# Optimization experiments

Hardware: AMD Instinct MI355X
Metric: run time of the kernel (lower is better)

Reference implementation:

```python
import jax, jax.numpy as jnp
import numpy as np

N = 50000
E = 800000
EP = 200000
IN_C = 128
HID = 128


def setup_inputs() -> dict:
    key = jax.random.key(0)
    ks = jax.random.split(key, 10)
    x = jax.random.normal(ks[0], (N, IN_C), dtype=jnp.float32)
    edge_index = jax.random.randint(ks[1], (2, E), 0, N, dtype=jnp.int64)
    pred_edges = jax.random.randint(ks[2], (2, EP), 0, N, dtype=jnp.int64)
    s_in = 1.0 / np.sqrt(IN_C)
    s_h = 1.0 / np.sqrt(HID)
    W1l = jax.random.normal(ks[3], (IN_C, HID), dtype=jnp.float32) * s_in
    W1r = jax.random.normal(ks[4], (IN_C, HID), dtype=jnp.float32) * s_in
    b1 = jnp.zeros((HID,), dtype=jnp.float32)
    W2l = jax.random.normal(ks[5], (HID, HID), dtype=jnp.float32) * s_h
    W2r = jax.random.normal(ks[6], (HID, HID), dtype=jnp.float32) * s_h
    b2 = jnp.zeros((HID,), dtype=jnp.float32)
    return {"x": x, "W1l": W1l, "b1": b1, "W1r": W1r,
            "W2l": W2l, "b2": b2, "W2r": W2r,
            "edge_index": edge_index, "pred_edges": pred_edges}


def _sage_conv(h, Wl, b, Wr, src, dst, n_nodes):
    # PyG SAGEConv (aggr='mean'): out = lin_l(mean_j x_j) + lin_r(x_i)
    msg = h[src]                                              # (E, D) gather
    agg = jax.ops.segment_sum(msg, dst, num_segments=n_nodes)  # (N, D) scatter-add
    deg = jax.ops.segment_sum(jnp.ones((src.shape[0],), h.dtype), dst,
                              num_segments=n_nodes)
    agg = agg / jnp.maximum(deg, 1.0)[:, None]                # mean (0 for isolated)
    return agg @ Wl + b + h @ Wr


def reference(x, W1l, b1, W1r, W2l, b2, W2r, edge_index, pred_edges):
    n_nodes = x.shape[0]
    src, dst = edge_index[0], edge_index[1]
    h = jax.nn.relu(_sage_conv(x, W1l, b1, W1r, src, dst, n_nodes))
    z = _sage_conv(h, W2l, b2, W2r, src, dst, n_nodes)
    ps, pd = pred_edges[0], pred_edges[1]
    return jnp.sum(z[ps] * z[pd], axis=-1)  # (E_pred,) logits
```

## Files before the change

kernel.cpp:

```cpp
#include <hip/hip_runtime.h>

#define D 128

typedef __attribute__((ext_vector_type(8))) short short8;
typedef __attribute__((ext_vector_type(4))) float f32x4;

__device__ inline unsigned int f2bf_bits(float f) {
    unsigned int u = __float_as_uint(f);
    return (u + 0x7FFFu + ((u >> 16) & 1u)) >> 16;
}

__device__ inline float bfhi(unsigned int u) { return __uint_as_float(u << 16); }
__device__ inline float bflo(unsigned int u) { return __uint_as_float(u & 0xffff0000u); }

__global__ __launch_bounds__(256) void prep_kernel(
    const float* __restrict__ x,
    const float* __restrict__ W1l, const float* __restrict__ W1r,
    const float* __restrict__ W2l, const float* __restrict__ W2r,
    const int* __restrict__ dst, int E,
    unsigned short* __restrict__ xbf, unsigned short* __restrict__ xlo,
    unsigned short* __restrict__ h1, unsigned short* __restrict__ l1,
    unsigned short* __restrict__ h2, unsigned short* __restrict__ l2,
    int n4, int ncast, int* __restrict__ chist2, int* __restrict__ csrpad)
{
    __shared__ int h[256];
    const int b = blockIdx.x;
    const int t = threadIdx.x;
    if (b < ncast) {
        int i = b * 256 + t;
        if (i >= n4) return;
        f32x4 v = *(const f32x4*)(x + (size_t)i * 4);
        ushort4 oh, ol;
        {
            unsigned int hb; float hf;
            hb = f2bf_bits(v.x); hf = __uint_as_float(hb << 16);
            oh.x = (unsigned short)hb; ol.x = (unsigned short)f2bf_bits(v.x - hf);
            hb = f2bf_bits(v.y); hf = __uint_as_float(hb << 16);
            oh.y = (unsigned short)hb; ol.y = (unsigned short)f2bf_bits(v.y - hf);
            hb = f2bf_bits(v.z); hf = __uint_as_float(hb << 16);
            oh.z = (unsigned short)hb; ol.z = (unsigned short)f2bf_bits(v.z - hf);
            hb = f2bf_bits(v.w); hf = __uint_as_float(hb << 16);
            oh.w = (unsigned short)hb; ol.w = (unsigned short)f2bf_bits(v.w - hf);
        }
        *(ushort4*)(xbf + (size_t)i * 4) = oh;
        *(ushort4*)(xlo + (size_t)i * 4) = ol;
    } else if (b < ncast + 256) {
        int gidx = (b - ncast) * 256 + t;
        int sel = gidx >> 15;
        int idx = gidx & 32767;
        int tt = idx >> 12;
        int ks = (idx >> 9) & 7;
        int lane = (idx >> 3) & 63;
        int j = idx & 7;
        int qq = lane >> 4, r16 = lane & 15;
        int k = ks * 32 + qq * 8 + j;
        int c = tt * 16 + r16;
        const float* Wl = sel ? W2l : W1l;
        const float* Wr = sel ? W2r : W1r;
        float v = (k < 128) ? Wl[k * 128 + c] : Wr[(k - 128) * 128 + c];
        unsigned int hb = f2bf_bits(v);
        float hf = __uint_as_float(hb << 16);
        unsigned int l = f2bf_bits(v - hf);
        (sel ? h2 : h1)[idx] = (unsigned short)hb;
        (sel ? l2 : l1)[idx] = (unsigned short)l;
    } else if (b < ncast + 512) {
        const int cb = b - ncast - 256;
        h[t] = 0;
        __syncthreads();
        for (int e = cb * 256 + t; e < E; e += 65536)
            atomicAdd(&h[dst[e] >> 8], 1);
        __syncthreads();
        chist2[cb * 256 + t] = h[t];
    } else {
        if (t < 32) csrpad[t] = 0;
    }
}

__global__ __launch_bounds__(256) void scan256_kernel(const int* __restrict__ chist2,
                                                      int* __restrict__ cbase,
                                                      int* __restrict__ gcur) {
    __shared__ int wsum[4];
    const int t = threadIdx.x, lane = t & 63, wv = t >> 6;
    int v = 0;
#pragma unroll 8
    for (int b = 0; b < 256; ++b) v += chist2[b * 256 + t];
    int s = v;
#pragma unroll
    for (int o = 1; o < 64; o <<= 1) {
        int u = __shfl_up(s, o, 64);
        if (lane >= o) s += u;
    }
    if (lane == 63) wsum[wv] = s;
    __syncthreads();
    int add = 0;
    for (int w = 0; w < wv; ++w) add += wsum[w];
    cbase[t + 1] = s + add;
    if (t == 0) cbase[0] = 0;
    gcur[t] = s + add - v;
}

#define CCHUNK 4096
__global__ __launch_bounds__(256) void coarse_scatter_kernel(
    const int* __restrict__ src, const int* __restrict__ dst,
    int* __restrict__ gcur, unsigned int* __restrict__ centries, int E)
{
    __shared__ int h[256];
    __shared__ int base[256];
    __shared__ unsigned int stage[CCHUNK];
    const int t = threadIdx.x;
    const int e0 = blockIdx.x * CCHUNK;
    h[t] = 0;
    __syncthreads();
#pragma unroll
    for (int i = 0; i < 16; ++i) {
        int e = e0 + i * 256 + t;
        unsigned int u = 0xFFFFFFFFu;
        if (e < E) {
            int d = dst[e];
            int s = src[e];
            int b = d >> 8;
            u = ((unsigned)b << 24) | ((unsigned)s << 8) | (unsigned)(d & 255);
            atomicAdd(&h[b], 1);
        }
        stage[i * 256 + t] = u;
    }
    __syncthreads();
    base[t] = atomicAdd(&gcur[t], h[t]);
    __syncthreads();
    h[t] = 0;
    __syncthreads();
#pragma unroll
    for (int i = 0; i < 16; ++i) {
        unsigned int u = stage[i * 256 + t];
        if (u != 0xFFFFFFFFu) {
            int b = u >> 24;
            int r = atomicAdd(&h[b], 1);
            centries[base[b] + r] = u & 0x00FFFFFFu;
        }
    }
}

#define DCAP 8192
__global__ __launch_bounds__(256) void fine_bucket_kernel(
    const unsigned int* __restrict__ centries,
    const int* __restrict__ cbase,
    int* __restrict__ offo, int* __restrict__ csr, int N, int E)
{
    __shared__ int h[256], ex[256], wsum[4];
    __shared__ int stg[DCAP];
    const int t = threadIdx.x, lane = t & 63, wv = t >> 6;
    const int b = blockIdx.x;
    const int s0 = cbase[b];
    const int cnt = cbase[b + 1] - s0;
    h[t] = 0;
    __syncthreads();
    for (int i = t; i < cnt; i += 256)
        atomicAdd(&h[centries[s0 + i] & 255], 1);
    __syncthreads();
    int v = h[t], s = v;
#pragma unroll
    for (int o = 1; o < 64; o <<= 1) {
        int u = __shfl_up(s, o, 64);
        if (lane >= o) s += u;
    }
    if (lane == 63) wsum[wv] = s;
    __syncthreads();
    int add = 0;
    for (int w = 0; w < wv; ++w) add += wsum[w];
    const int exc = s + add - v;
    ex[t] = exc;
    const int dg = b * 256 + t;
    if (dg < N) offo[dg] = s0 + exc;
    if (b == 0 && t == 0) offo[N] = E;
    h[t] = 0;
    __syncthreads();
    if (cnt <= DCAP) {
        for (int i = t; i < cnt; i += 256) {
            unsigned int u = centries[s0 + i];
            int dl = u & 255;
            int r = atomicAdd(&h[dl], 1);
            stg[ex[dl] + r] = (int)(u >> 8);
        }
        __syncthreads();
        for (int i = t; i < cnt; i += 256)
            csr[s0 + i] = stg[i];
    } else {
        for (int i = t; i < cnt; i += 256) {
            unsigned int u = centries[s0 + i];
            int dl = u & 255;
            int r = atomicAdd(&h[dl], 1);
            csr[s0 + ex[dl] + r] = (int)(u >> 8);
        }
    }
}

__global__ __launch_bounds__(256, 4) void fused_sage_kernel(
    const unsigned short* __restrict__ featbf,
    const int* __restrict__ off,
    const int* __restrict__ csr,
    const unsigned short* __restrict__ self_hi,
    const unsigned short* __restrict__ self_lo,
    const unsigned short* __restrict__ wpk_hi,
    const unsigned short* __restrict__ wpk_lo,
    const float* __restrict__ bias,
    unsigned short* __restrict__ out_hi,
    unsigned short* __restrict__ out_lo,
    int do_relu)
{
    __shared__ unsigned short AHs[4][64][8];
    __shared__ unsigned short ALs[4][64][8];
    __shared__ unsigned short outs_hi[16][128];
    __shared__ unsigned short outs_lo[16][128];

    const int w = threadIdx.x >> 6;
    const int l = threadIdx.x & 63;
    const int tile = blockIdx.x;
    const int n0w = tile * 16;

    const int gn = l >> 2;
    const int q2 = l & 3;
    const int gnode = n0w + gn;
    const int start = off[gnode];
    const int end   = off[gnode + 1];
    const unsigned short* fb = featbf + w * 32 + q2 * 8;

    float ga[8] = {0.f, 0.f, 0.f, 0.f, 0.f, 0.f, 0.f, 0.f};

#define ACC(rv)                                                         \
    { ga[0] += bfhi(rv.x); ga[1] += bflo(rv.x);                         \
      ga[2] += bfhi(rv.y); ga[3] += bflo(rv.y);                         \
      ga[4] += bfhi(rv.z); ga[5] += bflo(rv.z);                         \
      ga[6] += bfhi(rv.w); ga[7] += bflo(rv.w); }

    const uint4 zero4 = {0u, 0u, 0u, 0u};
    if (start < end) {
        int4 ix = *(const int4*)(csr + start);
        uint4 c0 = *(const uint4*)(fb + (size_t)ix.x * D);
        uint4 c1 = *(const uint4*)(fb + (size_t)ix.y * D);
        uint4 c2 = *(const uint4*)(fb + (size_t)ix.z * D);
        uint4 c3 = *(const uint4*)(fb + (size_t)ix.w * D);
        for (int e = start; e < end; e += 4) {
            int4 ixn = *(const int4*)(csr + e + 4);
            uint4 n0 = *(const uint4*)(fb + (size_t)ixn.x * D);
            uint4 n1 = *(const uint4*)(fb + (size_t)ixn.y * D);
            uint4 n2 = *(const uint4*)(fb + (size_t)ixn.z * D);
            uint4 n3 = *(const uint4*)(fb + (size_t)ixn.w * D);
            if (e + 1 >= end) c1 = zero4;
            if (e + 2 >= end) c2 = zero4;
            if (e + 3 >= end) c3 = zero4;
            ACC(c0) ACC(c1) ACC(c2) ACC(c3)
            c0 = n0; c1 = n1; c2 = n2; c3 = n3;
        }
    }
#undef ACC

    {
        const float dinv = 1.0f / (float)max(end - start, 1);
        short8 hi8, lo8;
#pragma unroll
        for (int c = 0; c < 8; ++c) {
            float v = ga[c] * dinv;
            unsigned int hb = f2bf_bits(v);
            hi8[c] = (short)hb;
            lo8[c] = (short)f2bf_bits(v - __uint_as_float(hb << 16));
        }
        *(short8*)&AHs[w][q2 * 16 + gn][0] = hi8;
        *(short8*)&ALs[w][q2 * 16 + gn][0] = lo8;
    }
    __syncthreads();

    const int q = l >> 4, r16 = l & 15;
    const int mnode = n0w + r16;
    f32x4 acc0 = {0.f, 0.f, 0.f, 0.f};
    f32x4 acc1 = {0.f, 0.f, 0.f, 0.f};
    const unsigned short* sph = self_hi + (size_t)mnode * D + q * 8;
    const unsigned short* spl = self_lo + (size_t)mnode * D + q * 8;
    const unsigned short* bh0 = wpk_hi + (size_t)(2 * w) * 4096 + l * 8;
    const unsigned short* bl0 = wpk_lo + (size_t)(2 * w) * 4096 + l * 8;

#pragma unroll
    for (int ks = 0; ks < 8; ++ks) {
        short8 AH, AL;
        if (ks < 4) {
            AH = *(const short8*)&AHs[ks][l][0];
            AL = *(const short8*)&ALs[ks][l][0];
        } else {
            AH = *(const short8*)(sph + (ks - 4) * 32);
            AL = *(const short8*)(spl + (ks - 4) * 32);
        }
        short8 BH0 = *(const short8*)(bh0 + ks * 512);
        short8 BL0 = *(const short8*)(bl0 + ks * 512);
        short8 BH1 = *(const short8*)(bh0 + 4096 + ks * 512);
        short8 BL1 = *(const short8*)(bl0 + 4096 + ks * 512);
        acc0 = __builtin_amdgcn_mfma_f32_16x16x32_bf16(AH, BH0, acc0, 0, 0, 0);
        acc0 = __builtin_amdgcn_mfma_f32_16x16x32_bf16(AL, BH0, acc0, 0, 0, 0);
        acc0 = __builtin_amdgcn_mfma_f32_16x16x32_bf16(AH, BL0, acc0, 0, 0, 0);
        acc1 = __builtin_amdgcn_mfma_f32_16x16x32_bf16(AH, BH1, acc1, 0, 0, 0);
        acc1 = __builtin_amdgcn_mfma_f32_16x16x32_bf16(AL, BH1, acc1, 0, 0, 0);
        acc1 = __builtin_amdgcn_mfma_f32_16x16x32_bf16(AH, BL1, acc1, 0, 0, 0);
    }

    {
        const float bv0 = bias[32 * w + r16];
        const float bv1 = bias[32 * w + 16 + r16];
#pragma unroll
        for (int r = 0; r < 4; ++r) {
            float v0 = acc0[r] + bv0;
            float v1 = acc1[r] + bv1;
            if (do_relu) { v0 = fmaxf(v0, 0.f); v1 = fmaxf(v1, 0.f); }
            const int row = q * 4 + r;
            unsigned int h0 = f2bf_bits(v0);
            unsigned int h1 = f2bf_bits(v1);
            outs_hi[row][32 * w + r16] = (unsigned short)h0;
            outs_hi[row][32 * w + 16 + r16] = (unsigned short)h1;
            outs_lo[row][32 * w + r16] =
                (unsigned short)f2bf_bits(v0 - __uint_as_float(h0 << 16));
            outs_lo[row][32 * w + 16 + r16] =
                (unsigned short)f2bf_bits(v1 - __uint_as_float(h1 << 16));
        }
    }
    __syncthreads();
    {
        const int tid = threadIdx.x;
        short8 vh = *(short8*)(&outs_hi[0][0] + tid * 8);
        *(short8*)(out_hi + (size_t)n0w * D + tid * 8) = vh;
        if (out_lo) {
            short8 vl = *(short8*)(&outs_lo[0][0] + tid * 8);
            *(short8*)(out_lo + (size_t)n0w * D + tid * 8) = vl;
        }
    }
}

__global__ __launch_bounds__(256) void pred_kernel(const unsigned short* __restrict__ zbf,
                                                   const int* __restrict__ ps,
                                                   const int* __restrict__ pd,
                                                   float* __restrict__ out, int EP) {
    int idx = blockIdx.x * 256 + threadIdx.x;
    int e = idx >> 4;
    if (e >= EP) return;
    int L = idx & 15;
    const unsigned short* fb = zbf + (size_t)L * 8;
    uint4 ra = *(const uint4*)(fb + (size_t)ps[e] * D);
    uint4 rb = *(const uint4*)(fb + (size_t)pd[e] * D);
    float p = bfhi(ra.x) * bfhi(rb.x) + bflo(ra.x) * bflo(rb.x)
            + bfhi(ra.y) * bfhi(rb.y) + bflo(ra.y) * bflo(rb.y)
            + bfhi(ra.z) * bfhi(rb.z) + bflo(ra.z) * bflo(rb.z)
            + bfhi(ra.w) * bfhi(rb.w) + bflo(ra.w) * bflo(rb.w);
#pragma unroll
    for (int off = 8; off > 0; off >>= 1) p += __shfl_xor(p, off, 16);
    if (L == 0) out[e] = p;
}

extern "C" void kernel_launch(void* const* d_in, const int* in_sizes, int n_in,
                              void* d_out, int out_size, void* d_ws, size_t ws_size,
                              hipStream_t stream) {
    const float* x   = (const float*)d_in[0];
    const float* W1l = (const float*)d_in[1];
    const float* b1  = (const float*)d_in[2];
    const float* W1r = (const float*)d_in[3];
    const float* W2l = (const float*)d_in[4];
    const float* b2  = (const float*)d_in[5];
    const float* W2r = (const float*)d_in[6];
    const int* edge_index = (const int*)d_in[7];
    const int* pred_edges = (const int*)d_in[8];
    float* out = (float*)d_out;

    const int N  = in_sizes[0] / D;
    const int E  = in_sizes[7] / 2;
    const int EP = in_sizes[8] / 2;

    const int* src = edge_index;
    const int* dst = edge_index + E;
    const int* ps  = pred_edges;
    const int* pd  = pred_edges + EP;

    int* chist2  = (int*)d_ws;
    int* cbase   = chist2 + 65536;
    int* gcur    = cbase + 272;
    int* off     = gcur + 256;
    unsigned int* centries = (unsigned int*)(off + 50016);
    int* csr     = (int*)(centries + E);
    unsigned short* w1_hi = (unsigned short*)(csr + E + 32 + 48);
    unsigned short* w1_lo = w1_hi + 32768;
    unsigned short* w2_hi = w1_lo + 32768;
    unsigned short* w2_lo = w2_hi + 32768;
    unsigned short* xbf   = w2_lo + 32768;
    unsigned short* xlo   = xbf + (size_t)N * D;
    unsigned short* hbf   = xlo + (size_t)N * D;
    unsigned short* hlo   = hbf + (size_t)N * D;
    unsigned short* zbf   = hlo + (size_t)N * D;

    const int n4 = N * D / 4;
    const int ncast = (n4 + 255) / 256;
    const int ntiles = N / 16;
    const int nbC = (E + CCHUNK - 1) / CCHUNK;
    const int nbD = (N + 255) / 256;
    const int nblk_pred = (EP * 16 + 255) / 256;

    prep_kernel<<<ncast + 513, 256, 0, stream>>>(x, W1l, W1r, W2l, W2r, dst, E,
                                                 xbf, xlo, w1_hi, w1_lo, w2_hi, w2_lo,
                                                 n4, ncast, chist2, csr + E);

    scan256_kernel<<<1, 256, 0, stream>>>(chist2, cbase, gcur);
    coarse_scatter_kernel<<<nbC, 256, 0, stream>>>(src, dst, gcur, centries, E);
    fine_bucket_kernel<<<nbD, 256, 0, stream>>>(centries, cbase, off, csr, N, E);

    fused_sage_kernel<<<ntiles, 256, 0, stream>>>(xbf, off, csr, xbf, xlo,
                                                  w1_hi, w1_lo, b1, hbf, hlo, 1);
    fused_sage_kernel<<<ntiles, 256, 0, stream>>>(hbf, off, csr, hbf, hlo,
                                                  w2_hi, w2_lo, b2, zbf,
                                                  (unsigned short*)nullptr, 0);
    pred_kernel<<<nblk_pred, 256, 0, stream>>>(zbf, ps, pd, out, EP);
}
```

Measured before the change: 241.3 us.

## Sort nodes by degree to balance neighbor-aggregation work within tiles

```diff
diff --git a/kernel.cpp b/kernel.cpp
--- a/kernel.cpp
+++ b/kernel.cpp
@@ -21,7 +21,8 @@
     unsigned short* __restrict__ xbf, unsigned short* __restrict__ xlo,
     unsigned short* __restrict__ h1, unsigned short* __restrict__ l1,
     unsigned short* __restrict__ h2, unsigned short* __restrict__ l2,
-    int n4, int ncast, int* __restrict__ chist2, int* __restrict__ csrpad)
+    int n4, int ncast, int* __restrict__ chist2, int* __restrict__ csrpad,
+    int* __restrict__ dhist)
 {
     __shared__ int h[256];
     const int b = blockIdx.x;
@@ -72,6 +73,7 @@
         __syncthreads();
         chist2[cb * 256 + t] = h[t];
     } else {
+        dhist[t] = 0;
         if (t < 32) csrpad[t] = 0;
     }
 }
@@ -144,7 +146,8 @@
 __global__ __launch_bounds__(256) void fine_bucket_kernel(
     const unsigned int* __restrict__ centries,
     const int* __restrict__ cbase,
-    int* __restrict__ offo, int* __restrict__ csr, int N, int E)
+    int* __restrict__ offo, int* __restrict__ csr,
+    int* __restrict__ deg, int* __restrict__ dhist, int N, int E)
 {
     __shared__ int h[256], ex[256], wsum[4];
     __shared__ int stg[DCAP];
@@ -158,6 +161,11 @@
         atomicAdd(&h[centries[s0 + i] & 255], 1);
     __syncthreads();
     int v = h[t], s = v;
+    const int dg = b * 256 + t;
+    if (dg < N) {
+        deg[dg] = v;
+        atomicAdd(&dhist[min(v, 255)], 1);
+    }
 #pragma unroll
     for (int o = 1; o < 64; o <<= 1) {
         int u = __shfl_up(s, o, 64);
@@ -169,7 +177,6 @@
     for (int w = 0; w < wv; ++w) add += wsum[w];
     const int exc = s + add - v;
     ex[t] = exc;
-    const int dg = b * 256 + t;
     if (dg < N) offo[dg] = s0 + exc;
     if (b == 0 && t == 0) offo[N] = E;
     h[t] = 0;
@@ -194,10 +201,39 @@
     }
 }
 
+__global__ __launch_bounds__(256) void dscan_kernel(const int* __restrict__ dhist,
+                                                    int* __restrict__ dcur) {
+    __shared__ int wsum[4];
+    const int t = threadIdx.x, lane = t & 63, wv = t >> 6;
+    int v = dhist[t];
+    int s = v;
+#pragma unroll
+    for (int o = 1; o < 64; o <<= 1) {
+        int u = __shfl_up(s, o, 64);
+        if (lane >= o) s += u;
+    }
+    if (lane == 63) wsum[wv] = s;
+    __syncthreads();
+    int add = 0;
+    for (int w = 0; w < wv; ++w) add += wsum[w];
+    dcur[t] = s + add - v;
+}
+
+__global__ __launch_bounds__(256) void dperm_kernel(const int* __restrict__ deg,
+                                                    int* __restrict__ dcur,
+                                                    int* __restrict__ perm, int N) {
+    int n = blockIdx.x * 256 + threadIdx.x;
+    if (n >= N) return;
+    int d = min(deg[n], 255);
+    int pos = atomicAdd(&dcur[d], 1);
+    perm[pos] = n;
+}
+
 __global__ __launch_bounds__(256, 4) void fused_sage_kernel(
     const unsigned short* __restrict__ featbf,
     const int* __restrict__ off,
     const int* __restrict__ csr,
+    const int* __restrict__ perm,
     const unsigned short* __restrict__ self_hi,
     const unsigned short* __restrict__ self_lo,
     const unsigned short* __restrict__ wpk_hi,
@@ -219,7 +255,7 @@
 
     const int gn = l >> 2;
     const int q2 = l & 3;
-    const int gnode = n0w + gn;
+    const int gnode = perm[n0w + gn];
     const int start = off[gnode];
     const int end   = off[gnode + 1];
     const unsigned short* fb = featbf + w * 32 + q2 * 8;
@@ -270,7 +306,7 @@
     __syncthreads();
 
     const int q = l >> 4, r16 = l & 15;
-    const int mnode = n0w + r16;
+    const int mnode = perm[n0w + r16];
     f32x4 acc0 = {0.f, 0.f, 0.f, 0.f};
     f32x4 acc1 = {0.f, 0.f, 0.f, 0.f};
     const unsigned short* sph = self_hi + (size_t)mnode * D + q * 8;
@@ -322,11 +358,13 @@
     __syncthreads();
     {
         const int tid = threadIdx.x;
-        short8 vh = *(short8*)(&outs_hi[0][0] + tid * 8);
-        *(short8*)(out_hi + (size_t)n0w * D + tid * 8) = vh;
+        const int row = tid >> 4, ch = tid & 15;
+        const int dn = perm[n0w + row];
+        short8 vh = *(short8*)(&outs_hi[row][ch * 8]);
+        *(short8*)(out_hi + (size_t)dn * D + ch * 8) = vh;
         if (out_lo) {
-            short8 vl = *(short8*)(&outs_lo[0][0] + tid * 8);
-            *(short8*)(out_lo + (size_t)n0w * D + tid * 8) = vl;
+            short8 vl = *(short8*)(&outs_lo[row][ch * 8]);
+            *(short8*)(out_lo + (size_t)dn * D + ch * 8) = vl;
         }
     }
 }
@@ -378,7 +416,11 @@
     int* cbase   = chist2 + 65536;
     int* gcur    = cbase + 272;
     int* off     = gcur + 256;
-    unsigned int* centries = (unsigned int*)(off + 50016);
+    int* dhist   = off + 50016;
+    int* dcur    = dhist + 256;
+    int* deg     = dcur + 256;
+    int* perm    = deg + 50016;
+    unsigned int* centries = (unsigned int*)(perm + 50016);
     int* csr     = (int*)(centries + E);
     unsigned short* w1_hi = (unsigned short*)(csr + E + 32 + 48);
     unsigned short* w1_lo = w1_hi + 32768;
@@ -399,15 +441,19 @@
 
     prep_kernel<<<ncast + 513, 256, 0, stream>>>(x, W1l, W1r, W2l, W2r, dst, E,
                                                  xbf, xlo, w1_hi, w1_lo, w2_hi, w2_lo,
-                                                 n4, ncast, chist2, csr + E);
+                                                 n4, ncast, chist2, csr + E, dhist);
 
     scan256_kernel<<<1, 256, 0, stream>>>(chist2, cbase, gcur);
     coarse_scatter_kernel<<<nbC, 256, 0, stream>>>(src, dst, gcur, centries, E);
-    fine_bucket_kernel<<<nbD, 256, 0, stream>>>(centries, cbase, off, csr, N, E);
-
-    fused_sage_kernel<<<ntiles, 256, 0, stream>>>(xbf, off, csr, xbf, xlo,
+    fine_bucket_kernel<<<nbD, 256, 0, stream>>>(centries, cbase, off, csr,
+                                                deg, dhist, N, E);
+
+    dscan_kernel<<<1, 256, 0, stream>>>(dhist, dcur);
+    dperm_kernel<<<nbD, 256, 0, stream>>>(deg, dcur, perm, N);
+
+    fused_sage_kernel<<<ntiles, 256, 0, stream>>>(xbf, off, csr, perm, xbf, xlo,
                                                   w1_hi, w1_lo, b1, hbf, hlo, 1);
-    fused_sage_kernel<<<ntiles, 256, 0, stream>>>(hbf, off, csr, hbf, hlo,
+    fused_sage_kernel<<<ntiles, 256, 0, stream>>>(hbf, off, csr, perm, hbf, hlo,
                                                   w2_hi, w2_lo, b2, zbf,
                                                   (unsigned short*)nullptr, 0);
     pred_kernel<<<nblk_pred, 256, 0, stream>>>(zbf, ps, pd, out, EP);
```

New measurement: 462.3 us. 91.6% more time.
